# Optimization experiments

Measured on AMD Instinct MI355X. Metric: run time of the kernel, lower is better.

The kernel has to match this reference:

```python
import jax, jax.numpy as jnp
import numpy as np
from jax import lax

# Dims: c1=256, num_heads = c1//64 = 4, head_dim=64, key_dim=32 (attn_ratio=0.5)
B, C, H, W = 4, 256, 64, 64
NH, HD, KD = 4, 64, 32
HQKV = C + 2 * NH * KD  # 512
RED = 16  # channel-attention reduction


def setup_inputs() -> dict:
    key = jax.random.key(0)
    ks = jax.random.split(key, 11)
    s = 0.02
    return {
        "x": jax.random.normal(ks[0], (B, C, H, W), jnp.float32),
        # Attention params (Conv = conv+BN folded into conv+bias)
        "w_qkv": jax.random.normal(ks[1], (HQKV, C), jnp.float32) * s,   # 1x1 conv
        "b_qkv": jax.random.normal(ks[2], (HQKV,), jnp.float32) * s,
        "w_proj": jax.random.normal(ks[3], (C, C), jnp.float32) * s,     # 1x1 conv
        "b_proj": jax.random.normal(ks[4], (C,), jnp.float32) * s,
        "w_pe": jax.random.normal(ks[5], (C, 1, 3, 3), jnp.float32) * s, # depthwise 3x3
        "b_pe": jax.random.normal(ks[6], (C,), jnp.float32) * s,
        # ChannelAttention params (1x1 convs, no bias)
        "w_fc1": jax.random.normal(ks[7], (C // RED, C), jnp.float32) * s,
        "w_fc2": jax.random.normal(ks[8], (C, C // RED), jnp.float32) * s,
        # SpatialAttention conv (2->1 channels, 3x3, no bias)
        "w_sa": jax.random.normal(ks[9], (1, 2, 3, 3), jnp.float32) * s,
    }


def _conv1x1(x, w, b=None):
    y = jnp.einsum('bchw,oc->bohw', x, w)
    if b is not None:
        y = y + b[None, :, None, None]
    return y


def _dwconv3(x, w, b):
    y = lax.conv_general_dilated(
        x, w, window_strides=(1, 1), padding='SAME',
        feature_group_count=x.shape[1],
        dimension_numbers=('NCHW', 'OIHW', 'NCHW'))
    return y + b[None, :, None, None]


def reference(x, w_qkv, b_qkv, w_proj, b_proj, w_pe, b_pe, w_fc1, w_fc2, w_sa):
    Bb, Cc, Hh, Ww = x.shape
    N = Hh * Ww
    scale = KD ** -0.5

    # --- Attention (asymmetric q/k/v head dims) ---
    qkv = _conv1x1(x, w_qkv, b_qkv).reshape(Bb, NH, 2 * KD + HD, N)
    q = qkv[:, :, :KD]            # [B,h,KD,N]
    k = qkv[:, :, KD:2 * KD]      # [B,h,KD,N]
    v = qkv[:, :, 2 * KD:]        # [B,h,HD,N]
    attn = jnp.einsum('bhkn,bhkm->bhnm', q, k) * scale  # [B,h,N,N]
    attn = jax.nn.softmax(attn, axis=-1)
    out = jnp.einsum('bhdm,bhnm->bhdn', v, attn).reshape(Bb, Cc, Hh, Ww)
    out = out + _dwconv3(v.reshape(Bb, Cc, Hh, Ww), w_pe, b_pe)
    out = _conv1x1(out, w_proj, b_proj)
    x = x + out

    # --- Channel attention (shared MLP on avg+max pooled features) ---
    def mlp(u):  # u: [B,C]
        return jnp.maximum(u @ w_fc1.T, 0.0) @ w_fc2.T
    avg = jnp.mean(x, axis=(2, 3))
    mx = jnp.max(x, axis=(2, 3))
    ca = jax.nn.sigmoid(mlp(avg) + mlp(mx))[:, :, None, None]
    x = x * ca

    # --- Spatial attention ---
    sa_in = jnp.stack([jnp.mean(x, axis=1), jnp.max(x, axis=1)], axis=1)  # [B,2,H,W]
    sa = lax.conv_general_dilated(
        sa_in, w_sa, window_strides=(1, 1), padding='SAME',
        dimension_numbers=('NCHW', 'OIHW', 'NCHW'))
    sa = jax.nn.sigmoid(sa)
    return x * sa
```

## Files before the change

kernel.cpp:

```cpp
#include <hip/hip_runtime.h>
#include <hip/hip_bf16.h>

typedef __bf16 bf16;
typedef __bf16 bf16x4 __attribute__((ext_vector_type(4)));
typedef __bf16 bf16x8 __attribute__((ext_vector_type(8)));
typedef float f32x4 __attribute__((ext_vector_type(4)));

#define B_ 4
#define C_ 256
#define NH_ 4
#define KD_ 32
#define HD_ 64
#define N_ 4096
#define HQKV_ 512

__global__ __launch_bounds__(256) void k_convw(const float* wq, const float* wp,
                                               bf16* wqb, bf16* wpb) {
    int i = blockIdx.x * 256 + threadIdx.x;
    if (i < HQKV_ * C_) wqb[i] = (bf16)wq[i];
    if (i < C_ * C_)    wpb[i] = (bf16)wp[i];
}

__global__ __launch_bounds__(256) void k_transpose(const float* __restrict__ x,
                                                   bf16* __restrict__ xT) {
    __shared__ float tile[64][65];
    int b = blockIdx.z, c0 = blockIdx.y * 64, n0 = blockIdx.x * 64;
    int t = threadIdx.x;
    int lane = t & 63, wv = t >> 6;
    for (int k = 0; k < 16; ++k) {
        int cl = k * 4 + wv;
        tile[cl][lane] = x[((size_t)(b * C_ + c0 + cl)) * N_ + n0 + lane];
    }
    __syncthreads();
    for (int k = 0; k < 16; ++k) {
        int nl = k * 4 + wv;
        xT[((size_t)(b * N_ + n0 + nl)) * C_ + c0 + lane] = (bf16)tile[lane][nl];
    }
}

__global__ __launch_bounds__(256) void k_qkv(const bf16* __restrict__ wqb,
                                             const bf16* __restrict__ xT,
                                             const float* __restrict__ bias,
                                             bf16* __restrict__ qt, bf16* __restrict__ kt,
                                             bf16* __restrict__ vb) {
    int n0 = blockIdx.x * 64, o0 = blockIdx.y * 64, b = blockIdx.z;
    int t = threadIdx.x, w = t >> 6, l = t & 63, lr = l & 15, lg = l >> 4;
    const bf16* arow = wqb + (size_t)(o0 + 16 * w + lr) * C_ + 8 * lg;
    const bf16* brow = xT + ((size_t)b * N_ + n0 + lr) * C_ + 8 * lg;
    f32x4 acc[4];
    f32x4 zz = {0.f, 0.f, 0.f, 0.f};
    acc[0] = zz; acc[1] = zz; acc[2] = zz; acc[3] = zz;
    for (int kk = 0; kk < C_; kk += 32) {
        bf16x8 a = *(const bf16x8*)(arow + kk);
#pragma unroll
        for (int tt = 0; tt < 4; ++tt) {
            bf16x8 bb = *(const bf16x8*)(brow + (size_t)tt * 16 * C_ + kk);
            acc[tt] = __builtin_amdgcn_mfma_f32_16x16x32_bf16(a, bb, acc[tt], 0, 0, 0);
        }
    }
    const float scale = 0.25506953076085663f;
#pragma unroll
    for (int tt = 0; tt < 4; ++tt) {
        int n = n0 + 16 * tt + lr;
#pragma unroll
        for (int j = 0; j < 4; ++j) {
            int o = o0 + 16 * w + 4 * lg + j;
            float val = acc[tt][j] + bias[o];
            int h = o >> 7, r = o & 127;
            size_t bh = (size_t)(b * NH_ + h);
            if (r < KD_)            qt[(bh * N_ + n) * KD_ + r] = (bf16)(val * scale);
            else if (r < 2 * KD_)   kt[(bh * N_ + n) * KD_ + (r - KD_)] = (bf16)val;
            else                    vb[(bh * HD_ + (r - 2 * KD_)) * N_ + n] = (bf16)val;
        }
    }
}

__global__ __launch_bounds__(256, 3) void k_attn(const bf16* __restrict__ qt,
                                                 const bf16* __restrict__ kt,
                                                 const bf16* __restrict__ vb,
                                                 bf16* __restrict__ attnT) {
    __shared__ bf16 ldsK[2][64 * KD_];
    __shared__ bf16 ldsV[2][64 * 64];
    __shared__ float red[4096];
    int id = blockIdx.x;
    int bh = id & 15;
    int n0 = (id >> 4) * 64;
    int b = bh >> 2, h = bh & 3;
    int t = threadIdx.x, w = t >> 6, l = t & 63, lr = l & 15, lg = l >> 4;

    bf16x8 aq[4];
#pragma unroll
    for (int f = 0; f < 4; ++f)
        aq[f] = *(const bf16x8*)(qt + ((size_t)bh * N_ + n0 + 16 * f + lr) * KD_ + 8 * lg);

    int krow = 16 * w + (l >> 2);
    const bf16* kg = kt + ((size_t)bh * N_ + krow) * KD_ + 8 * (l & 3);
    int fkr = (krow ^ (krow >> 2)) & 3;
    int kwo = krow * KD_ + 8 * ((l & 3) ^ fkr);
    int vrow0 = 16 * w + (l >> 3), vrow1 = vrow0 + 8;
    const bf16* vg0 = vb + ((size_t)bh * HD_ + vrow0) * N_ + 8 * (l & 7);
    const bf16* vg1 = vb + ((size_t)bh * HD_ + vrow1) * N_ + 8 * (l & 7);
    int vwo0 = vrow0 * 64 + 8 * ((l & 7) ^ (vrow0 & 7));
    int vwo1 = vrow1 * 64 + 8 * ((l & 7) ^ (vrow1 & 7));

    int kro = (16 * w + lr) * KD_ + 8 * (lg ^ ((lr ^ (lr >> 2)) & 3));
    int vro = 8 * ((2 * w + (lg >> 1)) ^ (lr & 7)) + 4 * ((lg & 1) ^ ((lr >> 3) & 1));

    f32x4 zz = {0.f, 0.f, 0.f, 0.f};
    f32x4 oacc[4][4];
#pragma unroll
    for (int f = 0; f < 4; ++f)
#pragma unroll
        for (int dt = 0; dt < 4; ++dt) oacc[f][dt] = zz;
    float Lp[4] = {0.f, 0.f, 0.f, 0.f};

    bf16x8 rk  = *(const bf16x8*)(kg);
    bf16x8 rv0 = *(const bf16x8*)(vg0);
    bf16x8 rv1 = *(const bf16x8*)(vg1);

    int cur = 0;
    for (int m0 = 0; m0 < N_; m0 += 64, cur ^= 1) {
        *(bf16x8*)(&ldsK[cur][0] + kwo) = rk;
        *(bf16x8*)(&ldsV[cur][0] + vwo0) = rv0;
        *(bf16x8*)(&ldsV[cur][0] + vwo1) =
            __builtin_shufflevector(rv1, rv1, 4, 5, 6, 7, 0, 1, 2, 3);
        if (m0 + 64 < N_) {
            rk  = *(const bf16x8*)(kg + (size_t)(m0 + 64) * KD_);
            rv0 = *(const bf16x8*)(vg0 + m0 + 64);
            rv1 = *(const bf16x8*)(vg1 + m0 + 64);
        }
        __syncthreads();
        bf16x8 kf = *(const bf16x8*)(&ldsK[cur][0] + kro);
        bf16x4 vf[4];
#pragma unroll
        for (int dt = 0; dt < 4; ++dt)
            vf[dt] = *(const bf16x4*)(&ldsV[cur][0] + (16 * dt + lr) * 64 + vro);
#pragma unroll
        for (int f = 0; f < 4; ++f) {
            f32x4 s = __builtin_amdgcn_mfma_f32_16x16x32_bf16(kf, aq[f], zz, 0, 0, 0);
            f32x4 p;
#pragma unroll
            for (int j = 0; j < 4; ++j) p[j] = __builtin_amdgcn_exp2f(s[j]);
            Lp[f] += (p[0] + p[1]) + (p[2] + p[3]);
            bf16x4 pk;
#pragma unroll
            for (int j = 0; j < 4; ++j) pk[j] = (bf16)p[j];
#pragma unroll
            for (int dt = 0; dt < 4; ++dt)
                asm("s_nop 1\n\tv_mfma_f32_16x16x16_bf16 %0, %1, %2, %0"
                    : "+v"(oacc[f][dt]) : "v"(pk), "v"(vf[dt]));
        }
    }
    asm volatile("s_nop 7\n\ts_nop 7\n\ts_nop 7" ::: "memory");

#pragma unroll
    for (int f = 0; f < 4; ++f) {
        Lp[f] += __shfl_xor(Lp[f], 16);
        Lp[f] += __shfl_xor(Lp[f], 32);
    }
    if (lg == 0) {
#pragma unroll
        for (int f = 0; f < 4; ++f) red[w * 64 + 16 * f + lr] = Lp[f];
    }
    __syncthreads();
    float invL[4];
#pragma unroll
    for (int f = 0; f < 4; ++f) {
        float Lt = red[16 * f + lr] + red[64 + 16 * f + lr] +
                   red[128 + 16 * f + lr] + red[192 + 16 * f + lr];
        invL[f] = 1.f / Lt;
    }
    __syncthreads();

    f32x4 ofin[4];
#pragma unroll
    for (int f = 0; f < 4; ++f) ofin[f] = zz;
#pragma unroll
    for (int dt = 0; dt < 4; ++dt) {
#pragma unroll
        for (int f = 0; f < 4; ++f)
#pragma unroll
            for (int j = 0; j < 4; ++j)
                red[w * 1024 + (16 * f + 4 * lg + j) * 16 + lr] = oacc[f][dt][j];
        __syncthreads();
        if (w == dt) {
#pragma unroll
            for (int f = 0; f < 4; ++f)
#pragma unroll
                for (int j = 0; j < 4; ++j) {
                    int idx = (16 * f + 4 * lg + j) * 16 + lr;
                    ofin[f][j] = red[idx] + red[1024 + idx] + red[2048 + idx] + red[3072 + idx];
                }
        }
        __syncthreads();
    }

#pragma unroll
    for (int f = 0; f < 4; ++f) {
#pragma unroll
        for (int j = 0; j < 4; ++j) {
            float iv = __shfl(invL[f], 4 * lg + j);
            int n = n0 + 16 * f + 4 * lg + j;
            attnT[((size_t)b * N_ + n) * C_ + h * HD_ + 16 * w + lr] =
                (bf16)(ofin[f][j] * iv);
        }
    }
}

__global__ __launch_bounds__(256) void k_pe_add(const bf16* __restrict__ attnT,
                                                const bf16* __restrict__ vb,
                                                const float* __restrict__ wpe,
                                                const float* __restrict__ bpe,
                                                bf16* __restrict__ yT) {
    __shared__ float vt[64 * 199];
    int hh = blockIdx.x, c0 = blockIdx.y * 64, b = blockIdx.z;
    int t = threadIdx.x, lane = t & 63, wg = t >> 6;

    if (t < 192) {
        int c_l = t >> 2, kh2 = t & 3;
        if (kh2 < 3) {
            vt[c_l * 199 + kh2 * 66 + 0] = 0.f;
            vt[c_l * 199 + kh2 * 66 + 65] = 0.f;
        }
    }
    if (t >= 192) {
        int u = t - 192;
        int c_l = 48 + (u >> 2), kh2 = u & 3;
        if (kh2 < 3) {
            vt[c_l * 199 + kh2 * 66 + 0] = 0.f;
            vt[c_l * 199 + kh2 * 66 + 65] = 0.f;
        }
    }
#pragma unroll
    for (int kh = 0; kh < 3; ++kh) {
        int hh2 = hh + kh - 1;
        bool ok = (hh2 >= 0 && hh2 < 64);
        for (int ci = 0; ci < 16; ++ci) {
            int c_l = wg * 16 + ci;
            float val = ok ? (float)vb[((size_t)(b * C_ + c0 + c_l)) * N_ + hh2 * 64 + lane] : 0.f;
            vt[c_l * 199 + kh * 66 + 1 + lane] = val;
        }
    }
    __syncthreads();

    int c = c0 + lane;
    float w9[9];
#pragma unroll
    for (int k = 0; k < 9; ++k) w9[k] = wpe[c * 9 + k];
    float bc = bpe[c];
    const float* vrow = vt + lane * 199;

#pragma unroll
    for (int wi = 0; wi < 16; ++wi) {
        int w = wg * 16 + wi;
        float acc = bc;
#pragma unroll
        for (int kh = 0; kh < 3; ++kh)
#pragma unroll
            for (int kw = 0; kw < 3; ++kw)
                acc += vrow[kh * 66 + w + kw] * w9[kh * 3 + kw];
        int n = hh * 64 + w;
        size_t idx = ((size_t)b * N_ + n) * C_ + c;
        yT[idx] = (bf16)((float)attnT[idx] + acc);
    }
}

__global__ __launch_bounds__(256) void k_proj(const bf16* __restrict__ wpb,
                                              const bf16* __restrict__ yT,
                                              const float* __restrict__ bias,
                                              const float* __restrict__ x,
                                              float* __restrict__ x2) {
    int n0 = blockIdx.x * 64, o0 = blockIdx.y * 64, b = blockIdx.z;
    int t = threadIdx.x, w = t >> 6, l = t & 63, lr = l & 15, lg = l >> 4;
    const bf16* arow = wpb + (size_t)(o0 + 16 * w + lr) * C_ + 8 * lg;
    const bf16* brow = yT + ((size_t)b * N_ + n0 + lr) * C_ + 8 * lg;
    f32x4 acc[4];
    f32x4 zz = {0.f, 0.f, 0.f, 0.f};
    acc[0] = zz; acc[1] = zz; acc[2] = zz; acc[3] = zz;
    for (int kk = 0; kk < C_; kk += 32) {
        bf16x8 a = *(const bf16x8*)(arow + kk);
#pragma unroll
        for (int tt = 0; tt < 4; ++tt) {
            bf16x8 bb = *(const bf16x8*)(brow + (size_t)tt * 16 * C_ + kk);
            acc[tt] = __builtin_amdgcn_mfma_f32_16x16x32_bf16(a, bb, acc[tt], 0, 0, 0);
        }
    }
#pragma unroll
    for (int tt = 0; tt < 4; ++tt) {
        int n = n0 + 16 * tt + lr;
#pragma unroll
        for (int j = 0; j < 4; ++j) {
            int o = o0 + 16 * w + 4 * lg + j;
            size_t idx = ((size_t)b * C_ + o) * N_ + n;
            x2[idx] = x[idx] + acc[tt][j] + bias[o];
        }
    }
}

__global__ __launch_bounds__(256) void k_ca_red(const float* __restrict__ x2,
                                                float* __restrict__ avg, float* __restrict__ mx) {
    int bc = blockIdx.x;
    int t = threadIdx.x;
    const float* row = x2 + (size_t)bc * N_;
    float s = 0.f, m = -1e30f;
    for (int i = t; i < N_; i += 256) { float v = row[i]; s += v; m = fmaxf(m, v); }
#pragma unroll
    for (int d = 1; d < 64; d <<= 1) { s += __shfl_xor(s, d); m = fmaxf(m, __shfl_xor(m, d)); }
    __shared__ float ss[4], sm[4];
    int w = t >> 6;
    if ((t & 63) == 0) { ss[w] = s; sm[w] = m; }
    __syncthreads();
    if (t == 0) {
        avg[bc] = (ss[0] + ss[1] + ss[2] + ss[3]) / (float)N_;
        mx[bc] = fmaxf(fmaxf(sm[0], sm[1]), fmaxf(sm[2], sm[3]));
    }
}

__global__ __launch_bounds__(256) void k_ca_mlp(const float* __restrict__ avg,
                                                const float* __restrict__ mx,
                                                const float* __restrict__ wfc1,
                                                const float* __restrict__ wfc2,
                                                float* __restrict__ ca) {
    int b = blockIdx.x, t = threadIdx.x;
    __shared__ float hsum[16];
    if (t < 16) {
        const float* w1 = wfc1 + t * C_;
        float ha = 0.f, hm = 0.f;
        for (int c = 0; c < C_; ++c) { ha += avg[b * C_ + c] * w1[c]; hm += mx[b * C_ + c] * w1[c]; }
        hsum[t] = fmaxf(ha, 0.f) + fmaxf(hm, 0.f);
    }
    __syncthreads();
    float o = 0.f;
    const float* w2 = wfc2 + t * 16;
#pragma unroll
    for (int r = 0; r < 16; ++r) o += hsum[r] * w2[r];
    ca[b * C_ + t] = 1.f / (1.f + __expf(-o));
}

__global__ __launch_bounds__(256) void k_sa_red(const float* __restrict__ x2,
                                                const float* __restrict__ ca,
                                                float* __restrict__ sain) {
    int b = blockIdx.y;
    int n = blockIdx.x * 256 + threadIdx.x;
    __shared__ float cal[C_];
    cal[threadIdx.x] = ca[b * C_ + threadIdx.x];
    __syncthreads();
    float s = 0.f, m = -1e30f;
    for (int c = 0; c < C_; ++c) {
        float v = x2[((size_t)b * C_ + c) * N_ + n] * cal[c];
        s += v; m = fmaxf(m, v);
    }
    sain[((size_t)b * 2 + 0) * N_ + n] = s * (1.f / C_);
    sain[((size_t)b * 2 + 1) * N_ + n] = m;
}

__global__ __launch_bounds__(256) void k_final(const float* __restrict__ x2,
                                               const float* __restrict__ ca,
                                               const float* __restrict__ sain,
                                               const float* __restrict__ wsa,
                                               float* __restrict__ out) {
    int b = blockIdx.y;
    int n = blockIdx.x * 256 + threadIdx.x;
    __shared__ float cal[C_];
    cal[threadIdx.x] = ca[b * C_ + threadIdx.x];
    __syncthreads();
    int hh = n >> 6, ww = n & 63;
    float acc = 0.f;
#pragma unroll
    for (int i = 0; i < 2; ++i)
#pragma unroll
        for (int kh = 0; kh < 3; ++kh) {
            int hh2 = hh + kh - 1;
            if (hh2 < 0 || hh2 >= 64) continue;
#pragma unroll
            for (int kw = 0; kw < 3; ++kw) {
                int ww2 = ww + kw - 1;
                if (ww2 < 0 || ww2 >= 64) continue;
                acc += sain[((size_t)b * 2 + i) * N_ + hh2 * 64 + ww2] * wsa[i * 9 + kh * 3 + kw];
            }
        }
    float sa = 1.f / (1.f + __expf(-acc));
    for (int c = 0; c < C_; ++c) {
        size_t idx = ((size_t)b * C_ + c) * N_ + n;
        out[idx] = x2[idx] * cal[c] * sa;
    }
}

extern "C" void kernel_launch(void* const* d_in, const int* in_sizes, int n_in,
                              void* d_out, int out_size, void* d_ws, size_t ws_size,
                              hipStream_t stream) {
    const float* x     = (const float*)d_in[0];
    const float* wqkv  = (const float*)d_in[1];
    const float* bqkv  = (const float*)d_in[2];
    const float* wproj = (const float*)d_in[3];
    const float* bproj = (const float*)d_in[4];
    const float* wpe   = (const float*)d_in[5];
    const float* bpe   = (const float*)d_in[6];
    const float* wfc1  = (const float*)d_in[7];
    const float* wfc2  = (const float*)d_in[8];
    const float* wsa   = (const float*)d_in[9];
    float* out = (float*)d_out;

    char* ws = (char*)d_ws;
    size_t off = 0;
    auto alloc = [&](size_t bytes) {
        char* p = ws + off;
        off += (bytes + 255) & ~(size_t)255;
        return p;
    };
    bf16*  qt    = (bf16*)alloc((size_t)B_ * NH_ * N_ * KD_ * 2);
    bf16*  ktb   = (bf16*)alloc((size_t)B_ * NH_ * N_ * KD_ * 2);
    bf16*  vbuf  = (bf16*)alloc((size_t)B_ * NH_ * HD_ * N_ * 2);
    bf16*  xT    = (bf16*)alloc((size_t)B_ * N_ * C_ * 2);
    bf16*  attnT = (bf16*)alloc((size_t)B_ * N_ * C_ * 2);
    float* x2    = (float*)alloc((size_t)B_ * C_ * N_ * 4);
    bf16*  wqb   = (bf16*)alloc((size_t)HQKV_ * C_ * 2);
    bf16*  wpb   = (bf16*)alloc((size_t)C_ * C_ * 2);
    float* avg   = (float*)alloc(B_ * C_ * 4);
    float* mxb   = (float*)alloc(B_ * C_ * 4);
    float* cab   = (float*)alloc(B_ * C_ * 4);
    float* sain  = (float*)alloc((size_t)B_ * 2 * N_ * 4);
    bf16*  yT    = xT;

    k_convw<<<dim3((HQKV_ * C_ + 255) / 256), 256, 0, stream>>>(wqkv, wproj, wqb, wpb);
    k_transpose<<<dim3(64, 4, B_), 256, 0, stream>>>(x, xT);
    k_qkv<<<dim3(64, 8, B_), 256, 0, stream>>>(wqb, xT, bqkv, qt, ktb, vbuf);
    k_attn<<<dim3(1024), 256, 0, stream>>>(qt, ktb, vbuf, attnT);
    k_pe_add<<<dim3(64, 4, B_), 256, 0, stream>>>(attnT, vbuf, wpe, bpe, yT);
    k_proj<<<dim3(64, 4, B_), 256, 0, stream>>>(wpb, yT, bproj, x, x2);
    k_ca_red<<<dim3(B_ * C_), 256, 0, stream>>>(x2, avg, mxb);
    k_ca_mlp<<<dim3(B_), 256, 0, stream>>>(avg, mxb, wfc1, wfc2, cab);
    k_sa_red<<<dim3(16, B_), 256, 0, stream>>>(x2, cab, sain);
    k_final<<<dim3(16, B_), 256, 0, stream>>>(x2, cab, sain, wsa, out);
}
```

Before: 229.3 us.

## Fuse channel pooling into projection, store x2 in bf16, shrink attention LDS

The projection kernel now emits per-block partial sums and maxima for channel attention. This replaces the separate full-tensor reduction kernel with a small finalize kernel that also runs the MLP. The intermediate x2 is stored in bf16 instead of fp32, halving traffic for the two later passes at the cost of precision. The attention kernel aliases its reduction buffer onto the K/V staging LDS to raise occupancy to 4 blocks per CU, adding a barrier, and groups the four PV MFMAs into one asm block with a single nop.

```diff
diff --git a/kernel.cpp b/kernel.cpp
--- a/kernel.cpp
+++ b/kernel.cpp
@@ -75,13 +75,14 @@
     }
 }
 
-__global__ __launch_bounds__(256, 3) void k_attn(const bf16* __restrict__ qt,
+__global__ __launch_bounds__(256, 4) void k_attn(const bf16* __restrict__ qt,
                                                  const bf16* __restrict__ kt,
                                                  const bf16* __restrict__ vb,
                                                  bf16* __restrict__ attnT) {
-    __shared__ bf16 ldsK[2][64 * KD_];
-    __shared__ bf16 ldsV[2][64 * 64];
-    __shared__ float red[4096];
+    __shared__ char smem[24576];
+    bf16* ldsK = (bf16*)smem;
+    bf16* ldsV = (bf16*)(smem + 8192);
+    float* red = (float*)smem;
     int id = blockIdx.x;
     int bh = id & 15;
     int n0 = (id >> 4) * 64;
@@ -120,9 +121,9 @@
 
     int cur = 0;
     for (int m0 = 0; m0 < N_; m0 += 64, cur ^= 1) {
-        *(bf16x8*)(&ldsK[cur][0] + kwo) = rk;
-        *(bf16x8*)(&ldsV[cur][0] + vwo0) = rv0;
-        *(bf16x8*)(&ldsV[cur][0] + vwo1) =
+        *(bf16x8*)(ldsK + cur * (64 * KD_) + kwo) = rk;
+        *(bf16x8*)(ldsV + cur * (64 * 64) + vwo0) = rv0;
+        *(bf16x8*)(ldsV + cur * (64 * 64) + vwo1) =
             __builtin_shufflevector(rv1, rv1, 4, 5, 6, 7, 0, 1, 2, 3);
         if (m0 + 64 < N_) {
             rk  = *(const bf16x8*)(kg + (size_t)(m0 + 64) * KD_);
@@ -130,11 +131,11 @@
             rv1 = *(const bf16x8*)(vg1 + m0 + 64);
         }
         __syncthreads();
-        bf16x8 kf = *(const bf16x8*)(&ldsK[cur][0] + kro);
+        bf16x8 kf = *(const bf16x8*)(ldsK + cur * (64 * KD_) + kro);
         bf16x4 vf[4];
 #pragma unroll
         for (int dt = 0; dt < 4; ++dt)
-            vf[dt] = *(const bf16x4*)(&ldsV[cur][0] + (16 * dt + lr) * 64 + vro);
+            vf[dt] = *(const bf16x4*)(ldsV + cur * (64 * 64) + (16 * dt + lr) * 64 + vro);
 #pragma unroll
         for (int f = 0; f < 4; ++f) {
             f32x4 s = __builtin_amdgcn_mfma_f32_16x16x32_bf16(kf, aq[f], zz, 0, 0, 0);
@@ -145,13 +146,17 @@
             bf16x4 pk;
 #pragma unroll
             for (int j = 0; j < 4; ++j) pk[j] = (bf16)p[j];
-#pragma unroll
-            for (int dt = 0; dt < 4; ++dt)
-                asm("s_nop 1\n\tv_mfma_f32_16x16x16_bf16 %0, %1, %2, %0"
-                    : "+v"(oacc[f][dt]) : "v"(pk), "v"(vf[dt]));
+            asm("s_nop 1\n\t"
+                "v_mfma_f32_16x16x16_bf16 %0, %4, %5, %0\n\t"
+                "v_mfma_f32_16x16x16_bf16 %1, %4, %6, %1\n\t"
+                "v_mfma_f32_16x16x16_bf16 %2, %4, %7, %2\n\t"
+                "v_mfma_f32_16x16x16_bf16 %3, %4, %8, %3"
+                : "+v"(oacc[f][0]), "+v"(oacc[f][1]), "+v"(oacc[f][2]), "+v"(oacc[f][3])
+                : "v"(pk), "v"(vf[0]), "v"(vf[1]), "v"(vf[2]), "v"(vf[3]));
         }
     }
     asm volatile("s_nop 7\n\ts_nop 7\n\ts_nop 7" ::: "memory");
+    __syncthreads();
 
 #pragma unroll
     for (int f = 0; f < 4; ++f) {
@@ -269,7 +274,9 @@
                                               const bf16* __restrict__ yT,
                                               const float* __restrict__ bias,
                                               const float* __restrict__ x,
-                                              float* __restrict__ x2) {
+                                              bf16* __restrict__ x2,
+                                              float* __restrict__ psum,
+                                              float* __restrict__ pmax) {
     int n0 = blockIdx.x * 64, o0 = blockIdx.y * 64, b = blockIdx.z;
     int t = threadIdx.x, w = t >> 6, l = t & 63, lr = l & 15, lg = l >> 4;
     const bf16* arow = wpb + (size_t)(o0 + 16 * w + lr) * C_ + 8 * lg;
@@ -285,6 +292,8 @@
             acc[tt] = __builtin_amdgcn_mfma_f32_16x16x32_bf16(a, bb, acc[tt], 0, 0, 0);
         }
     }
+    float lsum[4] = {0.f, 0.f, 0.f, 0.f};
+    float lmax[4] = {-1e30f, -1e30f, -1e30f, -1e30f};
 #pragma unroll
     for (int tt = 0; tt < 4; ++tt) {
         int n = n0 + 16 * tt + lr;
@@ -292,41 +301,51 @@
         for (int j = 0; j < 4; ++j) {
             int o = o0 + 16 * w + 4 * lg + j;
             size_t idx = ((size_t)b * C_ + o) * N_ + n;
-            x2[idx] = x[idx] + acc[tt][j] + bias[o];
-        }
-    }
-}
-
-__global__ __launch_bounds__(256) void k_ca_red(const float* __restrict__ x2,
-                                                float* __restrict__ avg, float* __restrict__ mx) {
-    int bc = blockIdx.x;
-    int t = threadIdx.x;
-    const float* row = x2 + (size_t)bc * N_;
-    float s = 0.f, m = -1e30f;
-    for (int i = t; i < N_; i += 256) { float v = row[i]; s += v; m = fmaxf(m, v); }
-#pragma unroll
-    for (int d = 1; d < 64; d <<= 1) { s += __shfl_xor(s, d); m = fmaxf(m, __shfl_xor(m, d)); }
-    __shared__ float ss[4], sm[4];
-    int w = t >> 6;
-    if ((t & 63) == 0) { ss[w] = s; sm[w] = m; }
-    __syncthreads();
-    if (t == 0) {
-        avg[bc] = (ss[0] + ss[1] + ss[2] + ss[3]) / (float)N_;
-        mx[bc] = fmaxf(fmaxf(sm[0], sm[1]), fmaxf(sm[2], sm[3]));
-    }
-}
-
-__global__ __launch_bounds__(256) void k_ca_mlp(const float* __restrict__ avg,
-                                                const float* __restrict__ mx,
+            float v = x[idx] + acc[tt][j] + bias[o];
+            x2[idx] = (bf16)v;
+            lsum[j] += v;
+            lmax[j] = fmaxf(lmax[j], v);
+        }
+    }
+#pragma unroll
+    for (int d = 1; d < 16; d <<= 1) {
+#pragma unroll
+        for (int j = 0; j < 4; ++j) {
+            lsum[j] += __shfl_xor(lsum[j], d);
+            lmax[j] = fmaxf(lmax[j], __shfl_xor(lmax[j], d));
+        }
+    }
+    if (lr == 0) {
+#pragma unroll
+        for (int j = 0; j < 4; ++j) {
+            int o = o0 + 16 * w + 4 * lg + j;
+            size_t pidx = ((size_t)(b * C_ + o)) * 64 + blockIdx.x;
+            psum[pidx] = lsum[j];
+            pmax[pidx] = lmax[j];
+        }
+    }
+}
+
+__global__ __launch_bounds__(256) void k_ca_fin(const float* __restrict__ psum,
+                                                const float* __restrict__ pmax,
                                                 const float* __restrict__ wfc1,
                                                 const float* __restrict__ wfc2,
                                                 float* __restrict__ ca) {
     int b = blockIdx.x, t = threadIdx.x;
+    const float* ps = psum + ((size_t)(b * C_ + t)) * 64;
+    const float* pm = pmax + ((size_t)(b * C_ + t)) * 64;
+    float s = 0.f, m = -1e30f;
+#pragma unroll 8
+    for (int i = 0; i < 64; ++i) { s += ps[i]; m = fmaxf(m, pm[i]); }
+    __shared__ float sav[C_], smx[C_];
+    sav[t] = s * (1.f / (float)N_);
+    smx[t] = m;
+    __syncthreads();
     __shared__ float hsum[16];
     if (t < 16) {
         const float* w1 = wfc1 + t * C_;
         float ha = 0.f, hm = 0.f;
-        for (int c = 0; c < C_; ++c) { ha += avg[b * C_ + c] * w1[c]; hm += mx[b * C_ + c] * w1[c]; }
+        for (int c = 0; c < C_; ++c) { ha += sav[c] * w1[c]; hm += smx[c] * w1[c]; }
         hsum[t] = fmaxf(ha, 0.f) + fmaxf(hm, 0.f);
     }
     __syncthreads();
@@ -337,7 +356,7 @@
     ca[b * C_ + t] = 1.f / (1.f + __expf(-o));
 }
 
-__global__ __launch_bounds__(256) void k_sa_red(const float* __restrict__ x2,
+__global__ __launch_bounds__(256) void k_sa_red(const bf16* __restrict__ x2,
                                                 const float* __restrict__ ca,
                                                 float* __restrict__ sain) {
     int b = blockIdx.y;
@@ -347,14 +366,14 @@
     __syncthreads();
     float s = 0.f, m = -1e30f;
     for (int c = 0; c < C_; ++c) {
-        float v = x2[((size_t)b * C_ + c) * N_ + n] * cal[c];
+        float v = (float)x2[((size_t)b * C_ + c) * N_ + n] * cal[c];
         s += v; m = fmaxf(m, v);
     }
     sain[((size_t)b * 2 + 0) * N_ + n] = s * (1.f / C_);
     sain[((size_t)b * 2 + 1) * N_ + n] = m;
 }
 
-__global__ __launch_bounds__(256) void k_final(const float* __restrict__ x2,
+__global__ __launch_bounds__(256) void k_final(const bf16* __restrict__ x2,
                                                const float* __restrict__ ca,
                                                const float* __restrict__ sain,
                                                const float* __restrict__ wsa,
@@ -382,7 +401,7 @@
     float sa = 1.f / (1.f + __expf(-acc));
     for (int c = 0; c < C_; ++c) {
         size_t idx = ((size_t)b * C_ + c) * N_ + n;
-        out[idx] = x2[idx] * cal[c] * sa;
+        out[idx] = (float)x2[idx] * cal[c] * sa;
     }
 }
 
@@ -413,11 +432,11 @@
     bf16*  vbuf  = (bf16*)alloc((size_t)B_ * NH_ * HD_ * N_ * 2);
     bf16*  xT    = (bf16*)alloc((size_t)B_ * N_ * C_ * 2);
     bf16*  attnT = (bf16*)alloc((size_t)B_ * N_ * C_ * 2);
-    float* x2    = (float*)alloc((size_t)B_ * C_ * N_ * 4);
+    bf16*  x2    = (bf16*)alloc((size_t)B_ * C_ * N_ * 2);
     bf16*  wqb   = (bf16*)alloc((size_t)HQKV_ * C_ * 2);
     bf16*  wpb   = (bf16*)alloc((size_t)C_ * C_ * 2);
-    float* avg   = (float*)alloc(B_ * C_ * 4);
-    float* mxb   = (float*)alloc(B_ * C_ * 4);
+    float* psum  = (float*)alloc((size_t)B_ * C_ * 64 * 4);
+    float* pmax  = (float*)alloc((size_t)B_ * C_ * 64 * 4);
     float* cab   = (float*)alloc(B_ * C_ * 4);
     float* sain  = (float*)alloc((size_t)B_ * 2 * N_ * 4);
     bf16*  yT    = xT;
@@ -427,9 +446,8 @@
     k_qkv<<<dim3(64, 8, B_), 256, 0, stream>>>(wqb, xT, bqkv, qt, ktb, vbuf);
     k_attn<<<dim3(1024), 256, 0, stream>>>(qt, ktb, vbuf, attnT);
     k_pe_add<<<dim3(64, 4, B_), 256, 0, stream>>>(attnT, vbuf, wpe, bpe, yT);
-    k_proj<<<dim3(64, 4, B_), 256, 0, stream>>>(wpb, yT, bproj, x, x2);
-    k_ca_red<<<dim3(B_ * C_), 256, 0, stream>>>(x2, avg, mxb);
-    k_ca_mlp<<<dim3(B_), 256, 0, stream>>>(avg, mxb, wfc1, wfc2, cab);
+    k_proj<<<dim3(64, 4, B_), 256, 0, stream>>>(wpb, yT, bproj, x, x2, psum, pmax);
+    k_ca_fin<<<dim3(B_), 256, 0, stream>>>(psum, pmax, wfc1, wfc2, cab);
     k_sa_red<<<dim3(16, B_), 256, 0, stream>>>(x2, cab, sain);
     k_final<<<dim3(16, B_), 256, 0, stream>>>(x2, cab, sain, wsa, out);
 }
```

New measurement: 243.4 us. 1.06x slower.
